# Optimization experiments

Hardware: AMD Instinct MI355X
Metric: run time of the kernel (lower is better)

## Reference

```python
import jax, jax.numpy as jnp
import numpy as np

H = 2048            # hidden_size
HK, HV = 16, 32     # num_k_heads, num_v_heads
DK, DV = 128, 128   # head dims
KEY_DIM = HK * DK   # 2048
VAL_DIM = HV * DV   # 4096
CONV_DIM = 2 * KEY_DIM + VAL_DIM  # 8192
KW = 4              # conv kernel width
CS = 64             # chunk size
B, S = 2, 4096
EPS = 1e-6


def setup_inputs() -> dict:
    key = jax.random.key(0)
    ks = jax.random.split(key, 8)
    sc = lambda n: 1.0 / np.sqrt(n)
    return {
        "hidden_states": jax.random.normal(ks[0], (B, S, H), jnp.float32),
        "W_qkvz": jax.random.normal(ks[1], (H, 2 * KEY_DIM + 2 * VAL_DIM), jnp.float32) * sc(H),
        "W_ba": jax.random.normal(ks[2], (H, 2 * HV), jnp.float32) * sc(H),
        "conv_w": jax.random.normal(ks[3], (CONV_DIM, KW), jnp.float32) * sc(KW),
        "A_log": jnp.log(jax.random.uniform(ks[4], (HV,), jnp.float32, 1.0, 16.0)),
        "dt_bias": jax.random.normal(ks[5], (HV,), jnp.float32) * 0.1,
        "norm_weight": jnp.ones((DV,), jnp.float32),
        "W_out": jax.random.normal(ks[6], (VAL_DIM, H), jnp.float32) * sc(VAL_DIM),
    }


def l2norm(x, eps=1e-6):
    return x * jax.lax.rsqrt(jnp.sum(x * x, -1, keepdims=True) + eps)


def chunk_gated_delta_rule(q, k, v, g, beta):
    # q,k: (B,S,HV,DK); v: (B,S,HV,DV); g,beta: (B,S,HV). S divisible by CS.
    q = l2norm(q)
    k = l2norm(k)
    tr = lambda x: jnp.swapaxes(x, 1, 2).astype(jnp.float32)  # -> (B,H,S,...)
    q, k, v = tr(q), tr(k), tr(v)
    g = jnp.swapaxes(g, 1, 2).astype(jnp.float32)
    beta = jnp.swapaxes(beta, 1, 2).astype(jnp.float32)
    q = q * (1.0 / np.sqrt(DK))
    nc = S // CS
    rs = lambda x: x.reshape(B, HV, nc, CS, x.shape[-1])
    v_beta = v * beta[..., None]
    k_beta = k * beta[..., None]
    q, k, v, k_beta, v_beta = map(rs, (q, k, v, k_beta, v_beta))
    g = jnp.cumsum(g.reshape(B, HV, nc, CS), -1)
    tril = jnp.tril(jnp.ones((CS, CS), bool))
    diff = g[..., :, None] - g[..., None, :]
    decay = jnp.exp(jnp.where(tril, diff, 0.0)) * tril  # (B,H,nc,CS,CS)
    # strictly-lower A; the original sequential loop computes T = (I - A)^{-1}
    A = -jnp.tril(jnp.einsum('bhcid,bhcjd->bhcij', k_beta, k) * decay, -1)
    eye = jnp.eye(CS, dtype=jnp.float32)
    T = jax.scipy.linalg.solve_triangular(
        eye - A, jnp.broadcast_to(eye, A.shape), lower=True, unit_diagonal=True)
    v_t = jnp.einsum('bhcij,bhcjd->bhcid', T, v_beta)
    k_cumdecay = jnp.einsum('bhcij,bhcjd->bhcid', T, k_beta * jnp.exp(g)[..., None])
    strict_low = jnp.tril(jnp.ones((CS, CS), jnp.float32), -1)

    def step(state, xs):
        q_i, k_i, v_i, kc_i, g_i, dm_i = xs  # (B,H,CS,*)
        attn = jnp.einsum('bhid,bhjd->bhij', q_i, k_i) * dm_i * strict_low
        v_new = v_i - kc_i @ state
        out = (q_i * jnp.exp(g_i)[..., None]) @ state + attn @ v_new
        g_last = g_i[..., -1]
        state = state * jnp.exp(g_last)[..., None, None] + jnp.einsum(
            'bhcd,bhcv->bhdv', k_i * jnp.exp(g_last[..., None] - g_i)[..., None], v_new)
        return state, out

    S0 = jnp.zeros((B, HV, DK, DV), jnp.float32)
    mv = lambda x: jnp.moveaxis(x, 2, 0)  # chunk axis first for scan
    _, outs = jax.lax.scan(step, S0, (mv(q), mv(k), mv(v_t), mv(k_cumdecay), mv(g), mv(decay)))
    out = jnp.moveaxis(outs, 0, 2).reshape(B, HV, S, DV)
    return jnp.swapaxes(out, 1, 2)  # (B,S,HV,DV)


def reference(hidden_states, W_qkvz, W_ba, conv_w, A_log, dt_bias, norm_weight, W_out):
    r = HV // HK
    qkvz = hidden_states @ W_qkvz                     # (B,S,2*KEY+2*VAL)
    ba = hidden_states @ W_ba                         # (B,S,2*HV)
    qkvz = qkvz.reshape(B, S, HK, 2 * DK + 2 * r * DV)
    q, k, v, z = jnp.split(qkvz, [DK, 2 * DK, 2 * DK + r * DV], axis=-1)
    v = v.reshape(B, S, HV, DV)
    z = z.reshape(B, S, HV, DV)
    ba = ba.reshape(B, S, HK, 2 * r)
    b, a = jnp.split(ba, [r], axis=-1)
    b = b.reshape(B, S, HV)
    a = a.reshape(B, S, HV)
    # fused causal depthwise conv + silu over [q|k|v]
    mixed = jnp.concatenate([q.reshape(B, S, -1), k.reshape(B, S, -1), v.reshape(B, S, -1)], -1)
    x = jnp.swapaxes(mixed, 1, 2)                     # (B, CONV_DIM, S)
    xp = jnp.pad(x, ((0, 0), (0, 0), (KW - 1, 0)))
    conv = sum(conv_w[:, j][None, :, None] * xp[:, :, j:j + S] for j in range(KW))
    conv = jax.nn.silu(conv)
    qkv = jnp.swapaxes(conv, 1, 2)
    q, k, v = jnp.split(qkv, [KEY_DIM, 2 * KEY_DIM], axis=-1)
    q = q.reshape(B, S, HK, DK)
    k = k.reshape(B, S, HK, DK)
    v = v.reshape(B, S, HV, DV)
    beta = jax.nn.sigmoid(b)
    g = -jnp.exp(A_log) * jax.nn.softplus(a + dt_bias)
    q = jnp.repeat(q, r, axis=2)
    k = jnp.repeat(k, r, axis=2)
    core = chunk_gated_delta_rule(q, k, v, g, beta)   # (B,S,HV,DV)
    # gated RMSNorm over head_v_dim
    cf = core.astype(jnp.float32)
    var = jnp.mean(cf * cf, -1, keepdims=True)
    core = cf * jax.lax.rsqrt(var + EPS) * norm_weight
    core = core * jax.nn.silu(z.astype(jnp.float32))
    return core.reshape(B, S, VAL_DIM) @ W_out        # (B,S,H)
```

## Files before the change

kernel.cpp:

```cpp
#include <hip/hip_runtime.h>
#include <cstdint>
#include <cstddef>


typedef _Float16 half_t;
typedef _Float16 half2_t __attribute__((ext_vector_type(2)));
typedef _Float16 half4_t __attribute__((ext_vector_type(4)));
typedef _Float16 half8   __attribute__((ext_vector_type(8)));
typedef float    f32x4   __attribute__((ext_vector_type(4)));

#define MFMA16(a, b, c) __builtin_amdgcn_mfma_f32_16x16x32_f16((a), (b), (c), 0, 0, 0)

#define AS1 __attribute__((address_space(1)))
#define AS3 __attribute__((address_space(3)))

__device__ __forceinline__ void gload16(void* lds, const void* g) {
    __builtin_amdgcn_global_load_lds((AS1 void*)(g), (AS3 void*)(lds), 16, 0, 0);
}

__device__ __forceinline__ void at_wr(float* AT, int i, int j, float v) {
    *(float*)((char*)AT + i * 256 + ((j * 4) ^ ((i & 7) << 4))) = v;
}
__device__ __forceinline__ half8 frag64(const half_t* base, int row, int koff) {
    return *(const half8*)((const char*)base + row * 128 + ((koff * 2) ^ ((row & 7) << 4)));
}
__device__ __forceinline__ void w64(half_t* base, int row, int col, float v) {
    *(half_t*)((char*)base + row * 128 + ((col * 2) ^ ((row & 7) << 4))) = (half_t)v;
}
__device__ __forceinline__ half8 frag128(const half_t* base, int row, int koff) {
    return *(const half8*)((const char*)base + row * 256 + ((koff * 2) ^ ((row & 7) << 4)));
}

__global__ __launch_bounds__(256) void cast_h_k(const float* __restrict__ src,
                                                half_t* __restrict__ dst) {
    const long n4 = (long)8192 * 2048 / 4;
    for (long i = (long)blockIdx.x * 256 + threadIdx.x; i < n4; i += (long)gridDim.x * 256) {
        f32x4 v = *(const f32x4*)(src + i * 4);
        half4_t h;
        h[0] = (half_t)v[0]; h[1] = (half_t)v[1]; h[2] = (half_t)v[2]; h[3] = (half_t)v[3];
        *(half4_t*)(dst + i * 4) = h;
    }
}

__global__ __launch_bounds__(256) void build_w1t_k(const float* __restrict__ Wq,
                                                   const float* __restrict__ Wba,
                                                   half_t* __restrict__ W1T) {
    __shared__ half_t tile[32][33];
    int n0 = blockIdx.x * 32, k0 = blockIdx.y * 32;
    int tx = threadIdx.x & 31, ty = threadIdx.x >> 5;
#pragma unroll
    for (int t = 0; t < 4; ++t) {
        int k = k0 + ty + t * 8, n = n0 + tx;
        float v = 0.f;
        if (n < 2048) {
            int kh = n >> 7, d = n & 127;
            v = Wq[(long)k * 12288 + kh * 768 + d];
        } else if (n < 4096) {
            int n2 = n - 2048; int kh = n2 >> 7, d = n2 & 127;
            v = Wq[(long)k * 12288 + kh * 768 + 128 + d];
        } else if (n < 8192) {
            int n3 = n - 4096; int vh = n3 >> 7, d = n3 & 127;
            int kh = vh >> 1, jj = vh & 1;
            v = Wq[(long)k * 12288 + kh * 768 + 256 + jj * 128 + d];
        } else if (n < 8256) {
            v = Wba[(long)k * 64 + (n - 8192)];
        } else if (n >= 8448) {
            int n4 = n - 8448; int vh = n4 >> 7, d = n4 & 127;
            int kh = vh >> 1, jj = vh & 1;
            v = Wq[(long)k * 12288 + kh * 768 + 512 + jj * 128 + d];
        }
        tile[ty + t * 8][tx] = (half_t)v;
    }
    __syncthreads();
#pragma unroll
    for (int t = 0; t < 4; ++t) {
        int n = n0 + ty + t * 8, k = k0 + tx;
        W1T[(long)n * 2048 + k] = tile[tx][ty + t * 8];
    }
}

__global__ __launch_bounds__(256) void build_wot_k(const float* __restrict__ Wo,
                                                   half_t* __restrict__ WoT) {
    __shared__ half_t tile[32][33];
    int n0 = blockIdx.x * 32, k0 = blockIdx.y * 32;
    int tx = threadIdx.x & 31, ty = threadIdx.x >> 5;
#pragma unroll
    for (int t = 0; t < 4; ++t) {
        int k = k0 + ty + t * 8, n = n0 + tx;
        tile[ty + t * 8][tx] = (half_t)Wo[(long)k * 2048 + n];
    }
    __syncthreads();
#pragma unroll
    for (int t = 0; t < 4; ++t) {
        int n = n0 + ty + t * 8, k = k0 + tx;
        WoT[(long)n * 4096 + k] = tile[tx][ty + t * 8];
    }
}

template <int OUT_F16>
__global__ __launch_bounds__(512, 2) void gemm256_k(const half_t* __restrict__ A,
                                                    const half_t* __restrict__ Bt,
                                                    void* __restrict__ C,
                                                    int K, int ldc,
                                                    int nwgM, int nwgN) {
    __shared__ half_t LA[2][2][8192];
    __shared__ half_t LB[2][2][8192];
    const int tid = threadIdx.x, lane = tid & 63, w = tid >> 6;
    const int lo = lane & 15, hi = lane >> 4;
    const int wm = w >> 2, wn = w & 3;
    const int nwg = gridDim.x, q = nwg >> 3, bid = blockIdx.x;
    const int swz = (bid & 7) * q + (bid >> 3);
    const int grp = 8 * nwgN;
    const int gid = swz / grp;
    const int rem = swz - gid * grp;
    const int fm = gid * 8;
    const int gsz = min(nwgM - fm, 8);
    const long tm = fm + rem % gsz;
    const long tn = rem / gsz;
    const long Kb = (long)K * 2;
    const char* Ab = (const char*)A + tm * 256 * Kb;
    const char* Bb = (const char*)Bt + tn * 256 * Kb;
    const int scol = ((lane & 7) << 4) ^ ((lane >> 3) << 4);
    const int srow = lane >> 3;
    const int s0 = w * 2, s1 = w * 2 + 1;

    auto stA = [&](int kt, int h) {
        char* hb = (char*)&LA[kt & 1][h][0];
        const char* gb = Ab + (long)(h * 128) * Kb + (long)kt * 128;
        gload16(hb + s0 * 1024, gb + (long)(s0 * 8 + srow) * Kb + scol);
        gload16(hb + s1 * 1024, gb + (long)(s1 * 8 + srow) * Kb + scol);
    };
    auto stB = [&](int kt, int h) {
        char* hb = (char*)&LB[kt & 1][h][0];
        const char* gb = Bb + (long)(h * 128) * Kb + (long)kt * 128;
        gload16(hb + s0 * 1024, gb + (long)(s0 * 8 + srow) * Kb + scol);
        gload16(hb + s1 * 1024, gb + (long)(s1 * 8 + srow) * Kb + scol);
    };
    auto stTile = [&](int kt) { stA(kt, 0); stA(kt, 1); stB(kt, 0); stB(kt, 1); };
    auto rdA = [&](int p, int mt, int ks) -> half8 {
        int r = mt * 16 + lo;
        return *(const half8*)((const char*)&LA[p][wm][0] + r * 128 +
                               ((ks * 64 + hi * 16) ^ ((r & 7) << 4)));
    };
    auto rdB = [&](int p, int nt, int ks) -> half8 {
        int r = (wn & 1) * 64 + nt * 16 + lo;
        return *(const half8*)((const char*)&LB[p][wn >> 1][0] + r * 128 +
                               ((ks * 64 + hi * 16) ^ ((r & 7) << 4)));
    };

    f32x4 acc[8][4] = {};
    half8 af[4][2], bfa[2][2], bfb[2][2];

    auto ldsA4 = [&](int p, int mbase) {
#pragma unroll
        for (int mt = 0; mt < 4; ++mt) {
            af[mt][0] = rdA(p, mbase + mt, 0);
            af[mt][1] = rdA(p, mbase + mt, 1);
        }
    };
    auto ldsB2 = [&](int p, int nbase, half8 (&dst)[2][2]) {
#pragma unroll
        for (int nt = 0; nt < 2; ++nt) {
            dst[nt][0] = rdB(p, nbase + nt, 0);
            dst[nt][1] = rdB(p, nbase + nt, 1);
        }
    };
    auto quad = [&](const half8 (&bq)[2][2], int mo, int no) {
        __builtin_amdgcn_s_setprio(1);
#pragma unroll
        for (int mt = 0; mt < 4; ++mt)
#pragma unroll
            for (int nt = 0; nt < 2; ++nt) {
                acc[mo + mt][no + nt] = MFMA16(af[mt][0], bq[nt][0], acc[mo + mt][no + nt]);
                acc[mo + mt][no + nt] = MFMA16(af[mt][1], bq[nt][1], acc[mo + mt][no + nt]);
            }
        __builtin_amdgcn_s_setprio(0);
    };

    const int nkt = K >> 6;
    stTile(0); stTile(1);
    asm volatile("s_waitcnt vmcnt(8)" ::: "memory");
    __builtin_amdgcn_s_barrier();
    ldsA4(0, 0); ldsB2(0, 0, bfa); ldsB2(0, 2, bfb);

    for (int kt = 0; kt < nkt; ++kt) {
        const int p = kt & 1;
        quad(bfa, 0, 0);
        quad(bfb, 0, 2);
        ldsA4(p, 4);
        quad(bfa, 4, 0);
        quad(bfb, 4, 2);
        __builtin_amdgcn_s_barrier();
        if (kt + 2 < nkt) {
            stTile(kt + 2);
            asm volatile("s_waitcnt vmcnt(8)" ::: "memory");
        } else if (kt + 1 < nkt) {
            asm volatile("s_waitcnt vmcnt(0)" ::: "memory");
        }
        __builtin_amdgcn_s_barrier();
        if (kt + 1 < nkt) {
            ldsA4(p ^ 1, 0);
            ldsB2(p ^ 1, 0, bfa);
            ldsB2(p ^ 1, 2, bfb);
        }
    }

    const long crow0 = tm * 256 + wm * 128 + hi * 4;
    const long ccol0 = tn * 256 + wn * 64 + lo;
#pragma unroll
    for (int mt = 0; mt < 8; ++mt)
#pragma unroll
        for (int nt = 0; nt < 4; ++nt)
#pragma unroll
            for (int e = 0; e < 4; ++e) {
                long row = crow0 + mt * 16 + e;
                long col = ccol0 + nt * 16;
                if (OUT_F16)
                    ((half_t*)C)[row * (long)ldc + col] = (half_t)acc[mt][nt][e];
                else
                    ((float*)C)[row * (long)ldc + col] = acc[mt][nt][e];
            }
}

__global__ __launch_bounds__(256) void conv_silu_k(const half_t* __restrict__ mixedH,
                                                   const float* __restrict__ conv_w,
                                                   half_t* __restrict__ qb,
                                                   half_t* __restrict__ kb,
                                                   half_t* __restrict__ vb) {
    const int ldm = 8448;
    int bx = blockIdx.x;
    int ch0 = (bx * 256 + threadIdx.x) * 8;
    int b = blockIdx.y >> 7, sc = blockIdx.y & 127;
    int s0 = sc * 32;
    half_t* dptr;
    long dstr;
    float nsc = 1.f;
    bool donorm = (bx < 2);
    if (bx == 0)      { dptr = qb + ch0;          dstr = 2048; nsc = 0.08838834764831845f; }
    else if (bx == 1) { dptr = kb + (ch0 - 2048); dstr = 2048; }
    else              { dptr = vb + (ch0 - 4096); dstr = 4096; }
    float w0[8], w1[8], w2[8], w3[8];
#pragma unroll
    for (int j = 0; j < 8; ++j) {
        f32x4 wv = *(const f32x4*)(conv_w + (ch0 + j) * 4);
        w0[j] = wv[0]; w1[j] = wv[1]; w2[j] = wv[2]; w3[j] = wv[3];
    }
    const half_t* src = mixedH + (long)b * 4096 * ldm + ch0;
    half8 x0 = {}, x1 = {}, x2 = {};
    if (s0 >= 3) {
        x0 = *(const half8*)(src + (long)(s0 - 3) * ldm);
        x1 = *(const half8*)(src + (long)(s0 - 2) * ldm);
        x2 = *(const half8*)(src + (long)(s0 - 1) * ldm);
    }
    for (int s = s0; s < s0 + 32; ++s) {
        half8 x3 = *(const half8*)(src + (long)s * ldm);
        float y[8];
        float ss = 0.f;
#pragma unroll
        for (int j = 0; j < 8; ++j) {
            float t = w0[j] * (float)x0[j] + w1[j] * (float)x1[j] +
                      w2[j] * (float)x2[j] + w3[j] * (float)x3[j];
            t = t / (1.f + __expf(-t));
            y[j] = t;
            ss += t * t;
        }
        half8 yv;
        if (donorm) {
            ss += __shfl_xor(ss, 1);
            ss += __shfl_xor(ss, 2);
            ss += __shfl_xor(ss, 4);
            ss += __shfl_xor(ss, 8);
            float r = rsqrtf(ss + 1e-6f) * nsc;
#pragma unroll
            for (int j = 0; j < 8; ++j) yv[j] = (half_t)(y[j] * r);
        } else {
#pragma unroll
            for (int j = 0; j < 8; ++j) yv[j] = (half_t)y[j];
        }
        *(half8*)(dptr + ((long)b * 4096 + s) * dstr) = yv;
        x0 = x1; x1 = x2; x2 = x3;
    }
}

__global__ __launch_bounds__(256) void gate_beta_k(const half_t* __restrict__ mixedH,
                                                   const float* __restrict__ A_log,
                                                   const float* __restrict__ dt_bias,
                                                   float* __restrict__ beta,
                                                   float* __restrict__ gcum) {
    __shared__ float gs[32][64];
    int b = blockIdx.x >> 6, c = blockIdx.x & 63;
    for (int idx = threadIdx.x; idx < 2048; idx += 256) {
        int vh = idx & 31, i = idx >> 5;
        int kh = vh >> 1, j = vh & 1;
        long row = ((long)b * 4096 + c * 64 + i) * 8448 + 8192 + kh * 4;
        float bb = (float)mixedH[row + j];
        float aa = (float)mixedH[row + 2 + j];
        beta[((long)b * 4096 + c * 64 + i) * 32 + vh] = 1.f / (1.f + __expf(-bb));
        float x = aa + dt_bias[vh];
        float sp = (x > 15.f) ? x : log1pf(__expf(x));
        gs[vh][i] = -__expf(A_log[vh]) * sp;
    }
    __syncthreads();
    if (threadIdx.x < 32) {
        int vh = threadIdx.x;
        float cum = 0.f;
        float* gout = gcum + ((long)(b * 32 + vh)) * 4096 + c * 64;
        for (int i = 0; i < 64; ++i) { cum += gs[vh][i]; gout[i] = cum; }
    }
}

__global__ __launch_bounds__(256) void phase1_k(const half_t* __restrict__ qb,
                                                const half_t* __restrict__ kb,
                                                const half_t* __restrict__ vb,
                                                const float* __restrict__ beta,
                                                const float* __restrict__ gcum,
                                                half_t* __restrict__ attnW,
                                                half_t* __restrict__ vtW,
                                                half_t* __restrict__ kcW) {
    __shared__ float AT[64 * 64];
    __shared__ half_t XT[256 * 64];
    __shared__ float gcS[64], betaS[64], egS[64];
    int blk = blockIdx.x;
    int c = blk & 63, vh = (blk >> 6) & 31, b = blk >> 11;
    int kh = vh >> 1;
    int tid = threadIdx.x, lane = tid & 63, w = tid >> 6, lo = lane & 15, hi = lane >> 4;
    long rowbase = (long)b * 4096 + c * 64;
    if (tid < 64) {
        float g = gcum[((long)(b * 32 + vh)) * 4096 + c * 64 + tid];
        gcS[tid] = g; egS[tid] = __expf(g);
        betaS[tid] = beta[(rowbase + tid) * 32 + vh];
    }
    const half_t* kR = kb + rowbase * 2048 + kh * 128;
    const half_t* qR = qb + rowbase * 2048 + kh * 128;
    f32x4 accG[4] = {}, accA[4] = {};
#pragma unroll
    for (int kt = 0; kt < 4; ++kt) {
        half8 ak = *(const half8*)(kR + (long)(w * 16 + lo) * 2048 + kt * 32 + hi * 8);
        half8 aq = *(const half8*)(qR + (long)(w * 16 + lo) * 2048 + kt * 32 + hi * 8);
#pragma unroll
        for (int n = 0; n < 4; ++n) {
            half8 bk = *(const half8*)(kR + (long)(n * 16 + lo) * 2048 + kt * 32 + hi * 8);
            accG[n] = MFMA16(ak, bk, accG[n]);
            accA[n] = MFMA16(aq, bk, accA[n]);
        }
    }
    __syncthreads();
    half_t* attnB = attnW + (long)blk * 4096;
#pragma unroll
    for (int n = 0; n < 4; ++n)
#pragma unroll
        for (int e = 0; e < 4; ++e) {
            int i = w * 16 + hi * 4 + e;
            int j = n * 16 + lo;
            float dec = (j < i) ? __expf(gcS[i] - gcS[j]) : 0.f;
            float av = (j < i) ? (-betaS[i] * accG[n][e] * dec) : (j == i ? 1.f : 0.f);
            at_wr(AT, i, j, av);
            attnB[(long)i * 64 + j] = (half_t)((j < i) ? accA[n][e] * dec : 0.f);
        }
    __syncthreads();
    if (w == 0) {
        float t[64];
#pragma unroll
        for (int i = 0; i < 64; ++i) t[i] = (lane == i) ? 1.f : 0.f;
#pragma unroll
        for (int i = 1; i < 64; ++i) {
            float a0 = 0.f, a1 = 0.f, a2 = 0.f, a3 = 0.f;
#pragma unroll
            for (int p0 = 0; p0 < i; p0 += 4) {
                f32x4 a4 = *(const f32x4*)((const char*)AT + i * 256 +
                                           ((p0 * 4) ^ ((i & 7) << 4)));
                if (p0 + 0 < i) a0 += a4[0] * t[p0 + 0];
                if (p0 + 1 < i) a1 += a4[1] * t[p0 + 1];
                if (p0 + 2 < i) a2 += a4[2] * t[p0 + 2];
                if (p0 + 3 < i) a3 += a4[3] * t[p0 + 3];
            }
            t[i] += (a0 + a1) + (a2 + a3);
        }
        half_t* TS = (half_t*)AT;
#pragma unroll
        for (int i = 0; i < 64; ++i)
            *(half_t*)((char*)TS + i * 128 + ((lane * 2) ^ ((i & 7) << 4))) = (half_t)t[i];
    } else {
        for (int idx = tid - 64; idx < 4096; idx += 192) {
            int p = idx >> 6, dp = idx & 63;
            float bb = betaS[p], be = betaS[p] * egS[p];
            half2_t vv = *(const half2_t*)(vb + (rowbase + p) * 4096 + vh * 128 + dp * 2);
            half2_t kk = *(const half2_t*)(kb + (rowbase + p) * 2048 + kh * 128 + dp * 2);
            w64(XT, dp * 2,       p, (float)vv[0] * bb);
            w64(XT, dp * 2 + 1,   p, (float)vv[1] * bb);
            w64(XT, 128 + dp * 2,     p, (float)kk[0] * be);
            w64(XT, 128 + dp * 2 + 1, p, (float)kk[1] * be);
        }
    }
    __syncthreads();
    const half_t* TS = (const half_t*)AT;
    f32x4 accO[4][4] = {};
#pragma unroll
    for (int kt = 0; kt < 2; ++kt) {
        half8 tf[4];
#pragma unroll
        for (int m = 0; m < 4; ++m) tf[m] = frag64(TS, m * 16 + lo, kt * 32 + hi * 8);
#pragma unroll
        for (int n = 0; n < 4; ++n) {
            half8 bx = frag64(XT, w * 64 + n * 16 + lo, kt * 32 + hi * 8);
#pragma unroll
            for (int m = 0; m < 4; ++m) accO[m][n] = MFMA16(tf[m], bx, accO[m][n]);
        }
    }
    long ob = (long)blk * 8192;
#pragma unroll
    for (int m = 0; m < 4; ++m)
#pragma unroll
        for (int n = 0; n < 4; ++n)
#pragma unroll
            for (int e = 0; e < 4; ++e) {
                int i = m * 16 + hi * 4 + e;
                int dc = w * 64 + n * 16 + lo;
                float v = accO[m][n][e];
                if (dc < 128) vtW[ob + (long)i * 128 + dc] = (half_t)v;
                else          kcW[ob + (long)i * 128 + dc - 128] = (half_t)(-v);
            }
}

struct P2Ops {
    half8 kcf[4], qf[4], k8[4];
    half8 atf[2];
    half_t vtv[8];
    float gm, gi, g63;
};

__global__ __launch_bounds__(256, 1) void phase2_k(const half_t* __restrict__ qb,
                                                   const half_t* __restrict__ kb,
                                                   const float* __restrict__ gcum,
                                                   const half_t* __restrict__ attnW,
                                                   const half_t* __restrict__ vtW,
                                                   const half_t* __restrict__ kcW,
                                                   half_t* __restrict__ coreH) {
    __shared__ half_t SHs[32 * 128];
    __shared__ half_t vnT[32 * 64];
    __shared__ half_t kdT[128 * 64];
    int blk = blockIdx.x;
    int bvh = blk & 63, js = blk >> 6;
    int vh = bvh & 31, b = bvh >> 5, kh = vh >> 1;
    int j0 = js * 32;
    int tid = threadIdx.x, lane = tid & 63, w = tid >> 6, lo = lane & 15, hi = lane >> 4;
    int ii = tid >> 2, dseg = tid & 3;
    int jm = w >> 1, dql = (w & 1) * 4;
    for (int idx = tid; idx < 32 * 128; idx += 256) SHs[idx] = (half_t)0.f;
    __syncthreads();
    const float* gbase = gcum + (long)bvh * 4096;

    auto loadops = [&](int c, P2Ops& o) {
        long pb = (long)bvh * 64 + c;
        const half_t* kcG = kcW + pb * 8192;
        const half_t* vtG = vtW + pb * 8192;
        const half_t* atG = attnW + pb * 4096;
        long rowbase = (long)b * 4096 + c * 64;
        const float* gp = gbase + c * 64;
#pragma unroll
        for (int kt = 0; kt < 4; ++kt) {
            o.kcf[kt] = *(const half8*)(kcG + (long)(w * 16 + lo) * 128 + kt * 32 + hi * 8);
            o.qf[kt] = *(const half8*)(qb + (rowbase + w * 16 + lo) * 2048 + kh * 128 +
                                       kt * 32 + hi * 8);
        }
#pragma unroll
        for (int kt2 = 0; kt2 < 2; ++kt2)
            o.atf[kt2] = *(const half8*)(atG + (long)(w * 16 + lo) * 64 + kt2 * 32 + hi * 8);
#pragma unroll
        for (int s = 0; s < 4; ++s)
            o.k8[s] = *(const half8*)(kb + (rowbase + ii) * 2048 + kh * 128 + dseg * 32 + s * 8);
#pragma unroll
        for (int n = 0; n < 2; ++n)
#pragma unroll
            for (int e = 0; e < 4; ++e)
                o.vtv[n * 4 + e] = vtG[(long)(w * 16 + hi * 4 + e) * 128 + j0 + n * 16 + lo];
        o.gm = gp[w * 16 + lo];
        o.gi = gp[ii];
        o.g63 = gp[63];
    };

    auto step = [&](int c, P2Ops& o, P2Ops& nx) {
        long rowbase = (long)b * 4096 + c * 64;
        loadops(c + 1 < 64 ? c + 1 : 63, nx);
        half8 bS[4][2];
#pragma unroll
        for (int kt = 0; kt < 4; ++kt) {
            bS[kt][0] = frag128(SHs, lo, kt * 32 + hi * 8);
            bS[kt][1] = frag128(SHs, 16 + lo, kt * 32 + hi * 8);
        }
        f32x4 accV[2];
#pragma unroll
        for (int n = 0; n < 2; ++n)
#pragma unroll
            for (int e = 0; e < 4; ++e) accV[n][e] = (float)o.vtv[n * 4 + e];
#pragma unroll
        for (int kt = 0; kt < 4; ++kt) {
            accV[0] = MFMA16(o.kcf[kt], bS[kt][0], accV[0]);
            accV[1] = MFMA16(o.kcf[kt], bS[kt][1], accV[1]);
        }
#pragma unroll
        for (int n = 0; n < 2; ++n) {
            int j = n * 16 + lo, i0 = w * 16 + hi * 4;
            half4_t h4;
            h4[0] = (half_t)accV[n][0]; h4[1] = (half_t)accV[n][1];
            h4[2] = (half_t)accV[n][2]; h4[3] = (half_t)accV[n][3];
            *(half4_t*)((char*)vnT + j * 128 + ((i0 * 2) ^ ((j & 7) << 4))) = h4;
        }
        {
            float ek = __expf(o.g63 - o.gi);
#pragma unroll
            for (int s = 0; s < 4; ++s)
#pragma unroll
                for (int e2 = 0; e2 < 8; ++e2)
                    w64(kdT, dseg * 32 + s * 8 + e2, ii, (float)o.k8[s][e2] * ek);
        }
        __syncthreads();
        float egm = __expf(o.gm);
        f32x4 accO[2] = {};
#pragma unroll
        for (int kt = 0; kt < 4; ++kt) {
            half8 aq;
#pragma unroll
            for (int e2 = 0; e2 < 8; ++e2) aq[e2] = (half_t)((float)o.qf[kt][e2] * egm);
            accO[0] = MFMA16(aq, bS[kt][0], accO[0]);
            accO[1] = MFMA16(aq, bS[kt][1], accO[1]);
        }
#pragma unroll
        for (int kt2 = 0; kt2 < 2; ++kt2) {
            half8 bV0 = frag64(vnT, lo, kt2 * 32 + hi * 8);
            half8 bV1 = frag64(vnT, 16 + lo, kt2 * 32 + hi * 8);
            accO[0] = MFMA16(o.atf[kt2], bV0, accO[0]);
            accO[1] = MFMA16(o.atf[kt2], bV1, accO[1]);
        }
        f32x4 accU[4] = {};
#pragma unroll
        for (int kt2 = 0; kt2 < 2; ++kt2) {
            half8 avn = frag64(vnT, jm * 16 + lo, kt2 * 32 + hi * 8);
#pragma unroll
            for (int dnn = 0; dnn < 4; ++dnn) {
                half8 bkd = frag64(kdT, (dql + dnn) * 16 + lo, kt2 * 32 + hi * 8);
                accU[dnn] = MFMA16(avn, bkd, accU[dnn]);
            }
        }
#pragma unroll
        for (int n = 0; n < 2; ++n)
#pragma unroll
            for (int e = 0; e < 4; ++e)
                coreH[(rowbase + w * 16 + hi * 4 + e) * 4096 + vh * 128 + j0 + n * 16 + lo] =
                    (half_t)accO[n][e];
        __syncthreads();
        float egl = __expf(o.g63);
#pragma unroll
        for (int dnn = 0; dnn < 4; ++dnn)
#pragma unroll
            for (int e = 0; e < 4; ++e) {
                int j = jm * 16 + hi * 4 + e;
                int d = (dql + dnn) * 16 + lo;
                char* p = (char*)SHs + j * 256 + ((d * 2) ^ ((j & 7) << 4));
                float old = (float)*(half_t*)p;
                *(half_t*)p = (half_t)(old * egl + accU[dnn][e]);
            }
        __syncthreads();
    };

    P2Ops opsA, opsB;
    loadops(0, opsA);
    for (int c = 0; c < 64; c += 2) {
        step(c, opsA, opsB);
        step(c + 1, opsB, opsA);
    }
}

__global__ __launch_bounds__(256) void normgate_k(half_t* __restrict__ coreH,
                                                  const half_t* __restrict__ zH,
                                                  const float* __restrict__ norm_w) {
    int w = threadIdx.x >> 6, lane = threadIdx.x & 63;
    float w0 = norm_w[lane * 2], w1 = norm_w[lane * 2 + 1];
    for (long rid = (long)blockIdx.x * 4 + w; rid < 262144; rid += (long)gridDim.x * 4) {
        long bs = rid >> 5;
        int vh = rid & 31;
        half_t* cr = coreH + bs * 4096 + vh * 128;
        half2_t cv = *(half2_t*)(cr + lane * 2);
        float f0 = (float)cv[0], f1 = (float)cv[1];
        float ss = f0 * f0 + f1 * f1;
#pragma unroll
        for (int off = 32; off; off >>= 1) ss += __shfl_xor(ss, off);
        float rs = rsqrtf(ss * (1.f / 128.f) + 1e-6f);
        half2_t zz = *(const half2_t*)(zH + bs * 4096 + vh * 128 + lane * 2);
        float z0 = (float)zz[0], z1 = (float)zz[1];
        float s0 = z0 / (1.f + __expf(-z0)), s1 = z1 / (1.f + __expf(-z1));
        half2_t o;
        o[0] = (half_t)(f0 * rs * w0 * s0);
        o[1] = (half_t)(f1 * rs * w1 * s1);
        *(half2_t*)(cr + lane * 2) = o;
    }
}

extern "C" void kernel_launch(void* const* d_in, const int* in_sizes, int n_in,
                              void* d_out, int out_size, void* d_ws, size_t ws_size,
                              hipStream_t stream) {
    const float* hidden  = (const float*)d_in[0];
    const float* W_qkvz  = (const float*)d_in[1];
    const float* W_ba    = (const float*)d_in[2];
    const float* conv_w  = (const float*)d_in[3];
    const float* A_log   = (const float*)d_in[4];
    const float* dt_bias = (const float*)d_in[5];
    const float* norm_w  = (const float*)d_in[6];
    const float* W_out   = (const float*)d_in[7];
    float* out = (float*)d_out;

    char* ws = (char*)d_ws;
    const size_t MB = 1ull << 20;
    half_t* qb      = (half_t*)(ws + 0);
    half_t* kb      = (half_t*)(ws + 32 * MB);
    half_t* vb      = (half_t*)(ws + 64 * MB);
    float*  betaB   = (float*) (ws + 128 * MB);
    float*  gcum    = (float*) (ws + 129 * MB);
    half_t* WoT     = (half_t*)(ws + 130 * MB);
    half_t* zH      = (half_t*)(ws + 146 * MB);
    half_t* mixedH  = (half_t*)(ws + 210 * MB);
    half_t* attnW   = (half_t*)(ws + 210 * MB);
    half_t* vtW     = (half_t*)(ws + 242 * MB);
    half_t* kcW     = (half_t*)(ws + 306 * MB);
    half_t* hiddenH = (half_t*)(ws + 0);
    half_t* W1T     = (half_t*)(ws + 32 * MB);
    half_t* coreH   = (half_t*)(ws + 64 * MB);
    (void)ws_size; (void)in_sizes; (void)n_in; (void)out_size;

    cast_h_k<<<2048, 256, 0, stream>>>(hidden, hiddenH);
    build_w1t_k<<<dim3(392, 64), 256, 0, stream>>>(W_qkvz, W_ba, W1T);
    build_wot_k<<<dim3(64, 128), 256, 0, stream>>>(W_out, WoT);
    gemm256_k<1><<<1056, 512, 0, stream>>>(hiddenH, W1T, mixedH, 2048, 8448, 32, 33);
    gemm256_k<1><<<512, 512, 0, stream>>>(hiddenH, W1T + (size_t)8448 * 2048, zH,
                                          2048, 4096, 32, 16);
    conv_silu_k<<<dim3(4, 256), 256, 0, stream>>>(mixedH, conv_w, qb, kb, vb);
    gate_beta_k<<<128, 256, 0, stream>>>(mixedH, A_log, dt_bias, betaB, gcum);
    phase1_k<<<4096, 256, 0, stream>>>(qb, kb, vb, betaB, gcum, attnW, vtW, kcW);
    phase2_k<<<256, 256, 0, stream>>>(qb, kb, gcum, attnW, vtW, kcW, coreH);
    normgate_k<<<4096, 256, 0, stream>>>(coreH, zH, norm_w);
    gemm256_k<0><<<256, 512, 0, stream>>>(coreH, WoT, out, 4096, 2048, 32, 8);
}
```

Before: 1.152 ms.

## Split 256x256 GEMM tile across 16 waves with 64x64 per-wave subtiles

The GEMM kernel now launches 1024 threads (16 waves) per workgroup instead of 512, and each wave computes a 64x64 output subtile instead of 128x64. The global-to-LDS staging is generalised so each wave loads two 8-row segments per operand. The register prefetch of the next LDS fragments is replaced by a simple per-k-chunk load-then-MFMA loop. The aim is more waves to hide latency, at the cost of lower per-wave register reuse. The tighter launch bound (1024,4) may also cap VGPRs and cause spills of the 64-float accumulator.

```diff
diff --git a/kernel.cpp b/kernel.cpp
--- a/kernel.cpp
+++ b/kernel.cpp
@@ -98,11 +98,11 @@
 }
 
 template <int OUT_F16>
-__global__ __launch_bounds__(512, 2) void gemm256_k(const half_t* __restrict__ A,
-                                                    const half_t* __restrict__ Bt,
-                                                    void* __restrict__ C,
-                                                    int K, int ldc,
-                                                    int nwgM, int nwgN) {
+__global__ __launch_bounds__(1024, 4) void gemm256_k(const half_t* __restrict__ A,
+                                                     const half_t* __restrict__ Bt,
+                                                     void* __restrict__ C,
+                                                     int K, int ldc,
+                                                     int nwgM, int nwgN) {
     __shared__ half_t LA[2][2][8192];
     __shared__ half_t LB[2][2][8192];
     const int tid = threadIdx.x, lane = tid & 63, w = tid >> 6;
@@ -122,93 +122,68 @@
     const char* Bb = (const char*)Bt + tn * 256 * Kb;
     const int scol = ((lane & 7) << 4) ^ ((lane >> 3) << 4);
     const int srow = lane >> 3;
-    const int s0 = w * 2, s1 = w * 2 + 1;
-
-    auto stA = [&](int kt, int h) {
-        char* hb = (char*)&LA[kt & 1][h][0];
-        const char* gb = Ab + (long)(h * 128) * Kb + (long)kt * 128;
-        gload16(hb + s0 * 1024, gb + (long)(s0 * 8 + srow) * Kb + scol);
-        gload16(hb + s1 * 1024, gb + (long)(s1 * 8 + srow) * Kb + scol);
+    const int sa0 = w * 2, sa1 = w * 2 + 1;
+
+    auto stSeg = [&](half_t (*L)[2][8192], const char* gb0, int kt, int s) {
+        int h = s >> 4, si = s & 15;
+        gload16((char*)&L[kt & 1][h][0] + si * 1024,
+                gb0 + (long)(h * 128 + si * 8 + srow) * Kb + (long)kt * 128 + scol);
     };
-    auto stB = [&](int kt, int h) {
-        char* hb = (char*)&LB[kt & 1][h][0];
-        const char* gb = Bb + (long)(h * 128) * Kb + (long)kt * 128;
-        gload16(hb + s0 * 1024, gb + (long)(s0 * 8 + srow) * Kb + scol);
-        gload16(hb + s1 * 1024, gb + (long)(s1 * 8 + srow) * Kb + scol);
+    auto stTile = [&](int kt) {
+        stSeg(LA, Ab, kt, sa0); stSeg(LA, Ab, kt, sa1);
+        stSeg(LB, Bb, kt, sa0); stSeg(LB, Bb, kt, sa1);
     };
-    auto stTile = [&](int kt) { stA(kt, 0); stA(kt, 1); stB(kt, 0); stB(kt, 1); };
-    auto rdA = [&](int p, int mt, int ks) -> half8 {
-        int r = mt * 16 + lo;
-        return *(const half8*)((const char*)&LA[p][wm][0] + r * 128 +
-                               ((ks * 64 + hi * 16) ^ ((r & 7) << 4)));
+    auto rdA = [&](int p, int mt, int kc) -> half8 {
+        int r = wm * 64 + mt * 16 + lo;
+        int rl = r & 127;
+        return *(const half8*)((const char*)&LA[p][r >> 7][0] + rl * 128 +
+                               ((kc * 64 + hi * 16) ^ ((rl & 7) << 4)));
     };
-    auto rdB = [&](int p, int nt, int ks) -> half8 {
-        int r = (wn & 1) * 64 + nt * 16 + lo;
-        return *(const half8*)((const char*)&LB[p][wn >> 1][0] + r * 128 +
-                               ((ks * 64 + hi * 16) ^ ((r & 7) << 4)));
+    auto rdB = [&](int p, int nt, int kc) -> half8 {
+        int r = wn * 64 + nt * 16 + lo;
+        int rl = r & 127;
+        return *(const half8*)((const char*)&LB[p][r >> 7][0] + rl * 128 +
+                               ((kc * 64 + hi * 16) ^ ((rl & 7) << 4)));
     };
 
-    f32x4 acc[8][4] = {};
-    half8 af[4][2], bfa[2][2], bfb[2][2];
-
-    auto ldsA4 = [&](int p, int mbase) {
-#pragma unroll
-        for (int mt = 0; mt < 4; ++mt) {
-            af[mt][0] = rdA(p, mbase + mt, 0);
-            af[mt][1] = rdA(p, mbase + mt, 1);
-        }
-    };
-    auto ldsB2 = [&](int p, int nbase, half8 (&dst)[2][2]) {
-#pragma unroll
-        for (int nt = 0; nt < 2; ++nt) {
-            dst[nt][0] = rdB(p, nbase + nt, 0);
-            dst[nt][1] = rdB(p, nbase + nt, 1);
-        }
-    };
-    auto quad = [&](const half8 (&bq)[2][2], int mo, int no) {
-        __builtin_amdgcn_s_setprio(1);
-#pragma unroll
-        for (int mt = 0; mt < 4; ++mt)
-#pragma unroll
-            for (int nt = 0; nt < 2; ++nt) {
-                acc[mo + mt][no + nt] = MFMA16(af[mt][0], bq[nt][0], acc[mo + mt][no + nt]);
-                acc[mo + mt][no + nt] = MFMA16(af[mt][1], bq[nt][1], acc[mo + mt][no + nt]);
-            }
-        __builtin_amdgcn_s_setprio(0);
-    };
+    f32x4 acc[4][4] = {};
 
     const int nkt = K >> 6;
     stTile(0); stTile(1);
-    asm volatile("s_waitcnt vmcnt(8)" ::: "memory");
+    asm volatile("s_waitcnt vmcnt(4)" ::: "memory");
     __builtin_amdgcn_s_barrier();
-    ldsA4(0, 0); ldsB2(0, 0, bfa); ldsB2(0, 2, bfb);
 
     for (int kt = 0; kt < nkt; ++kt) {
         const int p = kt & 1;
-        quad(bfa, 0, 0);
-        quad(bfb, 0, 2);
-        ldsA4(p, 4);
-        quad(bfa, 4, 0);
-        quad(bfb, 4, 2);
+#pragma unroll
+        for (int kc = 0; kc < 2; ++kc) {
+            half8 af[4], bf[4];
+#pragma unroll
+            for (int mt = 0; mt < 4; ++mt) af[mt] = rdA(p, mt, kc);
+#pragma unroll
+            for (int nt = 0; nt < 4; ++nt) bf[nt] = rdB(p, nt, kc);
+            __builtin_amdgcn_s_setprio(1);
+#pragma unroll
+            for (int mt = 0; mt < 4; ++mt)
+#pragma unroll
+                for (int nt = 0; nt < 4; ++nt)
+                    acc[mt][nt] = MFMA16(af[mt], bf[nt], acc[mt][nt]);
+            __builtin_amdgcn_s_setprio(0);
+        }
         __builtin_amdgcn_s_barrier();
         if (kt + 2 < nkt) {
             stTile(kt + 2);
-            asm volatile("s_waitcnt vmcnt(8)" ::: "memory");
+            asm volatile("s_waitcnt vmcnt(4)" ::: "memory");
         } else if (kt + 1 < nkt) {
             asm volatile("s_waitcnt vmcnt(0)" ::: "memory");
         }
         __builtin_amdgcn_s_barrier();
-        if (kt + 1 < nkt) {
-            ldsA4(p ^ 1, 0);
-            ldsB2(p ^ 1, 0, bfa);
-            ldsB2(p ^ 1, 2, bfb);
-        }
-    }
-
-    const long crow0 = tm * 256 + wm * 128 + hi * 4;
+    }
+
+    const long crow0 = tm * 256 + wm * 64 + hi * 4;
     const long ccol0 = tn * 256 + wn * 64 + lo;
 #pragma unroll
-    for (int mt = 0; mt < 8; ++mt)
+    for (int mt = 0; mt < 4; ++mt)
 #pragma unroll
         for (int nt = 0; nt < 4; ++nt)
 #pragma unroll
@@ -630,13 +605,13 @@
     cast_h_k<<<2048, 256, 0, stream>>>(hidden, hiddenH);
     build_w1t_k<<<dim3(392, 64), 256, 0, stream>>>(W_qkvz, W_ba, W1T);
     build_wot_k<<<dim3(64, 128), 256, 0, stream>>>(W_out, WoT);
-    gemm256_k<1><<<1056, 512, 0, stream>>>(hiddenH, W1T, mixedH, 2048, 8448, 32, 33);
-    gemm256_k<1><<<512, 512, 0, stream>>>(hiddenH, W1T + (size_t)8448 * 2048, zH,
-                                          2048, 4096, 32, 16);
+    gemm256_k<1><<<1056, 1024, 0, stream>>>(hiddenH, W1T, mixedH, 2048, 8448, 32, 33);
+    gemm256_k<1><<<512, 1024, 0, stream>>>(hiddenH, W1T + (size_t)8448 * 2048, zH,
+                                           2048, 4096, 32, 16);
     conv_silu_k<<<dim3(4, 256), 256, 0, stream>>>(mixedH, conv_w, qb, kb, vb);
     gate_beta_k<<<128, 256, 0, stream>>>(mixedH, A_log, dt_bias, betaB, gcum);
     phase1_k<<<4096, 256, 0, stream>>>(qb, kb, vb, betaB, gcum, attnW, vtW, kcW);
     phase2_k<<<256, 256, 0, stream>>>(qb, kb, gcum, attnW, vtW, kcW, coreH);
     normgate_k<<<4096, 256, 0, stream>>>(coreH, zH, norm_w);
-    gemm256_k<0><<<256, 512, 0, stream>>>(coreH, WoT, out, 4096, 2048, 32, 8);
-}
+    gemm256_k<0><<<256, 1024, 0, stream>>>(coreH, WoT, out, 4096, 2048, 32, 8);
+}
```

New measurement: 1.112 ms, median of 2. 1.04x faster.
